# Kernel tuning notes

Hardware: AMD Instinct MI355X
Metric: run time of the kernel (lower is better)

The kernel has to match this reference:

```python
import jax, jax.numpy as jnp
import numpy as np

B, IN, H = 4096, 1024, 1024

def setup_inputs() -> dict:
    key = jax.random.key(0)
    ks = jax.random.split(key, 8)
    s = 1.0 / np.sqrt(IN + H)  # ~torch Linear init scale
    return {
        "x": jax.random.normal(ks[0], (B, IN), jnp.float32),
        "h_prev": jax.random.normal(ks[1], (B, H), jnp.float32),
        "c_prev": jax.random.normal(ks[2], (B, H), jnp.float32),
        "Wf": jax.random.normal(ks[3], (IN + H, H), jnp.float32) * s,
        "bf": jnp.zeros((H,), jnp.float32),
        "Wi": jax.random.normal(ks[4], (IN + H, H), jnp.float32) * s,
        "bi": jnp.zeros((H,), jnp.float32),
        "Wg": jax.random.normal(ks[5], (IN + H, H), jnp.float32) * s,
        "bg": jnp.zeros((H,), jnp.float32),
        "Wo": jax.random.normal(ks[6], (IN + H, H), jnp.float32) * s,
        "bo": jnp.zeros((H,), jnp.float32),
    }

def reference(x, h_prev, c_prev, Wf, bf, Wi, bi, Wg, bg, Wo, bo):
    combined = jnp.concatenate([x, h_prev], axis=1)          # [B, IN+H]
    # fuse the 4 gate projections into one GEMM: [B, IN+H] x [IN+H, 4H]
    W = jnp.concatenate([Wf, Wi, Wg, Wo], axis=1)            # [IN+H, 4H]
    b = jnp.concatenate([bf, bi, bg, bo], axis=0)            # [4H]
    gates = combined @ W + b                                  # [B, 4H]
    f_t, i_t, g_t, o_t = jnp.split(gates, 4, axis=1)
    f_t = jax.nn.sigmoid(f_t)
    i_t = jax.nn.sigmoid(i_t)
    g_t = jnp.tanh(g_t)
    o_t = jax.nn.sigmoid(o_t)
    c_next = f_t * c_prev + i_t * g_t
    h_next = o_t * jnp.tanh(c_next)
    return (h_next, c_next)
```

## Files before the change

### kernel.cpp

```cpp
#include <hip/hip_runtime.h>

#define B_DIM 4096
#define H_DIM 1024
#define K_DIM 2048

typedef unsigned short u16;
typedef unsigned int u32;
typedef __attribute__((ext_vector_type(8))) short short8;
typedef __attribute__((ext_vector_type(4))) float f32x4;

typedef const __attribute__((address_space(1))) void* gas_ptr;
typedef __attribute__((address_space(3))) void* las_ptr;

#define WT_ELEMS (4 * H_DIM * K_DIM)
#define AC_ELEMS (B_DIM * K_DIM)
#define WS_NEEDED ((size_t)(WT_ELEMS + AC_ELEMS) * 2)

__device__ __forceinline__ void gl_lds16(const u16* g, u16* l) {
    __builtin_amdgcn_global_load_lds((gas_ptr)g, (las_ptr)l, 16, 0, 0);
}
__device__ __forceinline__ float bf2f(u16 v) {
    return __builtin_bit_cast(float, (u32)((u32)v << 16));
}
__device__ __forceinline__ u16 f2bf(float f) {
    u32 u = __builtin_bit_cast(u32, f);
    return (u16)((u + 0x7fffu + ((u >> 16) & 1u)) >> 16);
}
__device__ __forceinline__ float sigm(float x) { return 1.0f / (1.0f + __expf(-x)); }
__device__ __forceinline__ float tanh_f(float x) { return 1.0f - 2.0f / (__expf(2.0f * x) + 1.0f); }

__global__ __launch_bounds__(256) void prep_a(const float* __restrict__ x, const float* __restrict__ h,
                                              u16* __restrict__ A) {
    int gid = blockIdx.x * 256 + threadIdx.x;
    int e = gid * 8;
    int m = e >> 11, c = e & 2047;
    const float* src = (c < 1024) ? (x + (size_t)m * 1024 + c) : (h + (size_t)m * 1024 + (c - 1024));
    float4 v0 = ((const float4*)src)[0], v1 = ((const float4*)src)[1];
    short8 q;
    q[0] = (short)f2bf(v0.x); q[1] = (short)f2bf(v0.y); q[2] = (short)f2bf(v0.z); q[3] = (short)f2bf(v0.w);
    q[4] = (short)f2bf(v1.x); q[5] = (short)f2bf(v1.y); q[6] = (short)f2bf(v1.z); q[7] = (short)f2bf(v1.w);
    *(short8*)(A + e) = q;
}

__global__ __launch_bounds__(256) void prep_w(const float* __restrict__ Wf, const float* __restrict__ Wi,
                                              const float* __restrict__ Wg, const float* __restrict__ Wo,
                                              u16* __restrict__ Wt) {
    __shared__ u16 tl[64][72];
    const int t = threadIdx.x;
    const int k0 = blockIdx.x * 64, n0 = blockIdx.y * 64, g = blockIdx.z;
    const float* W = (g == 0) ? Wf : (g == 1) ? Wi : (g == 2) ? Wg : Wo;
    {
        int kl = t >> 2, nc = (t & 3) * 16;
        const float4* src = (const float4*)(W + (size_t)(k0 + kl) * H_DIM + n0 + nc);
        float4 v0 = src[0], v1 = src[1], v2 = src[2], v3 = src[3];
        short8 q0, q1;
        q0[0] = (short)f2bf(v0.x); q0[1] = (short)f2bf(v0.y); q0[2] = (short)f2bf(v0.z); q0[3] = (short)f2bf(v0.w);
        q0[4] = (short)f2bf(v1.x); q0[5] = (short)f2bf(v1.y); q0[6] = (short)f2bf(v1.z); q0[7] = (short)f2bf(v1.w);
        q1[0] = (short)f2bf(v2.x); q1[1] = (short)f2bf(v2.y); q1[2] = (short)f2bf(v2.z); q1[3] = (short)f2bf(v2.w);
        q1[4] = (short)f2bf(v3.x); q1[5] = (short)f2bf(v3.y); q1[6] = (short)f2bf(v3.z); q1[7] = (short)f2bf(v3.w);
        *(short8*)&tl[kl][nc] = q0;
        *(short8*)&tl[kl][nc + 8] = q1;
    }
    __syncthreads();
    {
        int nl = t >> 2, kc = (t & 3) * 16;
        short8 r0, r1;
#pragma unroll
        for (int j = 0; j < 8; ++j) { r0[j] = (short)tl[kc + j][nl]; r1[j] = (short)tl[kc + 8 + j][nl]; }
        u16* dst = Wt + (size_t)g * (H_DIM * K_DIM) + (size_t)(n0 + nl) * K_DIM + k0 + kc;
        *(short8*)dst = r0;
        *(short8*)(dst + 8) = r1;
    }
}

__global__ __launch_bounds__(256) void lstm_gemm(
    const u16* __restrict__ A, const u16* __restrict__ Wt, const float* __restrict__ c_prev,
    const float* __restrict__ bf_, const float* __restrict__ bi_,
    const float* __restrict__ bg_, const float* __restrict__ bo_,
    float* __restrict__ out) {
    __shared__ u16 sA[256 * 64];
    __shared__ u16 sB[4 * 16 * 64];

    const int t = threadIdx.x;
    const int w = t >> 6;
    const int l = t & 63;
    const int quad = l >> 4;
    const int l15 = l & 15;
    const int m0 = blockIdx.x * 256;
    const int j0 = blockIdx.y * 16;

    f32x4 acc[4][4];
#pragma unroll
    for (int g = 0; g < 4; ++g)
#pragma unroll
        for (int mi = 0; mi < 4; ++mi)
            acc[g][mi] = (f32x4){0.f, 0.f, 0.f, 0.f};

    const int v7 = l15 & 7;

    for (int kt = 0; kt < K_DIM / 64; ++kt) {
        __syncthreads();
#pragma unroll
        for (int i = 0; i < 8; ++i) {
            int c = i * 256 + t;
            int m = c >> 3, slot = c & 7;
            int k8 = (slot ^ (m & 7)) * 8;
            gl_lds16(A + (size_t)(m0 + m) * K_DIM + kt * 64 + k8, sA + c * 8);
        }
#pragma unroll
        for (int i = 0; i < 2; ++i) {
            int c = i * 256 + t;
            int g = c >> 7, r = c & 127;
            int n = r >> 3, slot = r & 7;
            int k8 = (slot ^ (n & 7)) * 8;
            gl_lds16(Wt + (size_t)g * (H_DIM * K_DIM) + (size_t)(j0 + n) * K_DIM + kt * 64 + k8,
                     sB + c * 8);
        }
        __syncthreads();

#pragma unroll
        for (int s = 0; s < 2; ++s) {
            const int sl = ((s * 4 + quad) ^ v7) * 8;
            short8 bfr[4];
#pragma unroll
            for (int g = 0; g < 4; ++g)
                bfr[g] = *(const short8*)(sB + g * 1024 + l15 * 64 + sl);
            short8 afr[4];
#pragma unroll
            for (int mi = 0; mi < 4; ++mi)
                afr[mi] = *(const short8*)(sA + (w * 64 + mi * 16 + l15) * 64 + sl);
#pragma unroll
            for (int g = 0; g < 4; ++g)
#pragma unroll
                for (int mi = 0; mi < 4; ++mi)
                    acc[g][mi] = __builtin_amdgcn_mfma_f32_16x16x32_bf16(afr[mi], bfr[g], acc[g][mi], 0, 0, 0);
        }
    }

    const int col = j0 + l15;
    const float bF = bf_[col], bI = bi_[col], bG = bg_[col], bO = bo_[col];
#pragma unroll
    for (int mi = 0; mi < 4; ++mi) {
        const int rowbase = m0 + w * 64 + mi * 16 + quad * 4;
        float cp[4];
#pragma unroll
        for (int rr = 0; rr < 4; ++rr)
            cp[rr] = c_prev[(size_t)(rowbase + rr) * H_DIM + col];
#pragma unroll
        for (int rr = 0; rr < 4; ++rr) {
            float fv = sigm(acc[0][mi][rr] + bF);
            float iv = sigm(acc[1][mi][rr] + bI);
            float gv = tanh_f(acc[2][mi][rr] + bG);
            float ov = sigm(acc[3][mi][rr] + bO);
            float cn = fv * cp[rr] + iv * gv;
            float hn = ov * tanh_f(cn);
            size_t idx = (size_t)(rowbase + rr) * H_DIM + col;
            out[idx] = hn;
            out[(size_t)B_DIM * H_DIM + idx] = cn;
        }
    }
}

__global__ __launch_bounds__(256) void lstm_f32(
    const float* __restrict__ x, const float* __restrict__ h_prev, const float* __restrict__ c_prev,
    const float* __restrict__ Wf, const float* __restrict__ Wi, const float* __restrict__ Wg, const float* __restrict__ Wo,
    const float* __restrict__ bf_, const float* __restrict__ bi_, const float* __restrict__ bg_, const float* __restrict__ bo_,
    float* __restrict__ out) {
    __shared__ u16 smem[16384];
    u16* sA = smem;
    u16* sB = smem + 4096;

    const int t = threadIdx.x;
    const int w = t >> 6;
    const int l = t & 63;
    const int quad = l >> 4;
    const int l15 = l & 15;
    const int wr = w >> 1;
    const int wc = w & 1;
    const int m0 = blockIdx.x * 128;
    const int j0 = blockIdx.y * 32;

    const int arow = t >> 1;
    const int akh = (t & 1) * 16;
    const int r7 = t & 127;
    const int bk = r7 >> 2;
    const int bn8 = (r7 & 3) * 8;
    const int kswz = ((((bk >> 3) ^ (bn8 >> 3)) << 3) | (bk & 7));
    const float* WpA = (t < 128) ? Wf : Wi;
    const float* WpB = (t < 128) ? Wg : Wo;
    const int gA = (t >> 7);
    const int gB = 2 + (t >> 7);

    f32x4 acc[2][4][2];
#pragma unroll
    for (int gi = 0; gi < 2; ++gi)
#pragma unroll
        for (int mi = 0; mi < 4; ++mi)
#pragma unroll
            for (int ni = 0; ni < 2; ++ni)
                acc[gi][mi][ni] = (f32x4){0.f, 0.f, 0.f, 0.f};

    for (int kt = 0; kt < K_DIM / 32; ++kt) {
        const float* srcA = (kt < 32) ? x : h_prev;
        const int koff = (kt & 31) * 32;
        __syncthreads();

        const float4* ap = (const float4*)(srcA + (size_t)(m0 + arow) * H_DIM + koff + akh);
        float4 a0 = ap[0], a1 = ap[1], a2 = ap[2], a3 = ap[3];
        short8 p0, p1;
        p0[0] = (short)f2bf(a0.x); p0[1] = (short)f2bf(a0.y); p0[2] = (short)f2bf(a0.z); p0[3] = (short)f2bf(a0.w);
        p0[4] = (short)f2bf(a1.x); p0[5] = (short)f2bf(a1.y); p0[6] = (short)f2bf(a1.z); p0[7] = (short)f2bf(a1.w);
        p1[0] = (short)f2bf(a2.x); p1[1] = (short)f2bf(a2.y); p1[2] = (short)f2bf(a2.z); p1[3] = (short)f2bf(a2.w);
        p1[4] = (short)f2bf(a3.x); p1[5] = (short)f2bf(a3.y); p1[6] = (short)f2bf(a3.z); p1[7] = (short)f2bf(a3.w);
        *(short8*)(sA + arow * 32 + akh) = p0;
        *(short8*)(sA + arow * 32 + akh + 8) = p1;

        const float* gpA = WpA + (size_t)(kt * 32 + bk) * H_DIM + j0 + bn8;
        const float* gpB = WpB + (size_t)(kt * 32 + bk) * H_DIM + j0 + bn8;
        float4 c0 = *(const float4*)gpA, c1 = *(const float4*)(gpA + 4);
        float4 d0 = *(const float4*)gpB, d1 = *(const float4*)(gpB + 4);
        sB[gA * 1024 + (bn8 + 0) * 32 + kswz] = f2bf(c0.x);
        sB[gA * 1024 + (bn8 + 1) * 32 + kswz] = f2bf(c0.y);
        sB[gA * 1024 + (bn8 + 2) * 32 + kswz] = f2bf(c0.z);
        sB[gA * 1024 + (bn8 + 3) * 32 + kswz] = f2bf(c0.w);
        sB[gA * 1024 + (bn8 + 4) * 32 + kswz] = f2bf(c1.x);
        sB[gA * 1024 + (bn8 + 5) * 32 + kswz] = f2bf(c1.y);
        sB[gA * 1024 + (bn8 + 6) * 32 + kswz] = f2bf(c1.z);
        sB[gA * 1024 + (bn8 + 7) * 32 + kswz] = f2bf(c1.w);
        sB[gB * 1024 + (bn8 + 0) * 32 + kswz] = f2bf(d0.x);
        sB[gB * 1024 + (bn8 + 1) * 32 + kswz] = f2bf(d0.y);
        sB[gB * 1024 + (bn8 + 2) * 32 + kswz] = f2bf(d0.z);
        sB[gB * 1024 + (bn8 + 3) * 32 + kswz] = f2bf(d0.w);
        sB[gB * 1024 + (bn8 + 4) * 32 + kswz] = f2bf(d1.x);
        sB[gB * 1024 + (bn8 + 5) * 32 + kswz] = f2bf(d1.y);
        sB[gB * 1024 + (bn8 + 6) * 32 + kswz] = f2bf(d1.z);
        sB[gB * 1024 + (bn8 + 7) * 32 + kswz] = f2bf(d1.w);
        __syncthreads();

        short8 bfr[2][2];
#pragma unroll
        for (int gi = 0; gi < 2; ++gi) {
            int g = wc * 2 + gi;
#pragma unroll
            for (int ni = 0; ni < 2; ++ni) {
                int n = ni * 16 + l15;
                bfr[gi][ni] = *(const short8*)(sB + g * 1024 + n * 32 + ((quad ^ (n >> 3)) * 8));
            }
        }
#pragma unroll
        for (int mi = 0; mi < 4; ++mi) {
            int m = wr * 64 + mi * 16 + l15;
            short8 afr = *(const short8*)(sA + m * 32 + quad * 8);
#pragma unroll
            for (int gi = 0; gi < 2; ++gi)
#pragma unroll
                for (int ni = 0; ni < 2; ++ni)
                    acc[gi][mi][ni] =
                        __builtin_amdgcn_mfma_f32_16x16x32_bf16(afr, bfr[gi][ni], acc[gi][mi][ni], 0, 0, 0);
        }
    }

    __syncthreads();
#pragma unroll
    for (int gi = 0; gi < 2; ++gi) {
        int g = wc * 2 + gi;
        const float* bp = (g == 0) ? bf_ : (g == 1) ? bi_ : (g == 2) ? bg_ : bo_;
#pragma unroll
        for (int ni = 0; ni < 2; ++ni) {
            int col = ni * 16 + l15;
            float bias = bp[j0 + col];
#pragma unroll
            for (int mi = 0; mi < 4; ++mi)
#pragma unroll
                for (int rr = 0; rr < 4; ++rr) {
                    int row = wr * 64 + mi * 16 + quad * 4 + rr;
                    float v = acc[gi][mi][ni][rr] + bias;
                    v = (g == 2) ? tanh_f(v) : sigm(v);
                    smem[g * 4096 + row * 32 + col] = f2bf(v);
                }
        }
    }
    __syncthreads();

    const int col = t & 31;
    const int rb = t >> 5;
#pragma unroll
    for (int p = 0; p < 16; ++p) {
        int row = p * 8 + rb;
        float fv = bf2f(smem[0 * 4096 + row * 32 + col]);
        float iv = bf2f(smem[1 * 4096 + row * 32 + col]);
        float gv = bf2f(smem[2 * 4096 + row * 32 + col]);
        float ov = bf2f(smem[3 * 4096 + row * 32 + col]);
        size_t oidx = (size_t)(m0 + row) * H_DIM + j0 + col;
        float cp = c_prev[oidx];
        float cn = fv * cp + iv * gv;
        float hn = ov * tanh_f(cn);
        out[oidx] = hn;
        out[(size_t)B_DIM * H_DIM + oidx] = cn;
    }
}

extern "C" void kernel_launch(void* const* d_in, const int* in_sizes, int n_in,
                              void* d_out, int out_size, void* d_ws, size_t ws_size,
                              hipStream_t stream) {
    const float* x   = (const float*)d_in[0];
    const float* hp  = (const float*)d_in[1];
    const float* cp  = (const float*)d_in[2];
    const float* Wf  = (const float*)d_in[3];
    const float* bf_ = (const float*)d_in[4];
    const float* Wi  = (const float*)d_in[5];
    const float* bi_ = (const float*)d_in[6];
    const float* Wg  = (const float*)d_in[7];
    const float* bg_ = (const float*)d_in[8];
    const float* Wo  = (const float*)d_in[9];
    const float* bo_ = (const float*)d_in[10];

    if (ws_size >= WS_NEEDED) {
        u16* Wt = (u16*)d_ws;
        u16* Ac = (u16*)d_ws + WT_ELEMS;
        prep_a<<<dim3(AC_ELEMS / 8 / 256), dim3(256), 0, stream>>>(x, hp, Ac);
        prep_w<<<dim3(K_DIM / 64, H_DIM / 64, 4), dim3(256), 0, stream>>>(Wf, Wi, Wg, Wo, Wt);
        lstm_gemm<<<dim3(B_DIM / 256, H_DIM / 16), dim3(256), 0, stream>>>(
            Ac, Wt, cp, bf_, bi_, bg_, bo_, (float*)d_out);
    } else {
        lstm_f32<<<dim3(B_DIM / 128, H_DIM / 32), dim3(256), 0, stream>>>(
            x, hp, cp, Wf, Wi, Wg, Wo, bf_, bi_, bg_, bo_, (float*)d_out);
    }
}
```

Baseline: 224.4 us.

## Reshape GEMM tile to 128x32 with 2x2 wave grid and merge prep kernels

The LSTM GEMM block tile changes from 256 rows x 16 columns per gate to 128 rows x 32 columns per gate, with the four waves arranged 2x2. This balances A and B reuse and lowers global/LDS traffic per output. Per-thread load pointers are precomputed and incremented each k-step, removing index arithmetic from the loop. The two conversion kernels for activations and weights are merged into one launch, cutting launch overhead and tail gaps.

```diff
diff --git a/kernel.cpp b/kernel.cpp
--- a/kernel.cpp
+++ b/kernel.cpp
@@ -29,47 +29,47 @@
 __device__ __forceinline__ float sigm(float x) { return 1.0f / (1.0f + __expf(-x)); }
 __device__ __forceinline__ float tanh_f(float x) { return 1.0f - 2.0f / (__expf(2.0f * x) + 1.0f); }
 
-__global__ __launch_bounds__(256) void prep_a(const float* __restrict__ x, const float* __restrict__ h,
-                                              u16* __restrict__ A) {
-    int gid = blockIdx.x * 256 + threadIdx.x;
-    int e = gid * 8;
-    int m = e >> 11, c = e & 2047;
-    const float* src = (c < 1024) ? (x + (size_t)m * 1024 + c) : (h + (size_t)m * 1024 + (c - 1024));
-    float4 v0 = ((const float4*)src)[0], v1 = ((const float4*)src)[1];
-    short8 q;
-    q[0] = (short)f2bf(v0.x); q[1] = (short)f2bf(v0.y); q[2] = (short)f2bf(v0.z); q[3] = (short)f2bf(v0.w);
-    q[4] = (short)f2bf(v1.x); q[5] = (short)f2bf(v1.y); q[6] = (short)f2bf(v1.z); q[7] = (short)f2bf(v1.w);
-    *(short8*)(A + e) = q;
-}
-
-__global__ __launch_bounds__(256) void prep_w(const float* __restrict__ Wf, const float* __restrict__ Wi,
-                                              const float* __restrict__ Wg, const float* __restrict__ Wo,
-                                              u16* __restrict__ Wt) {
+__global__ __launch_bounds__(256) void prep_all(const float* __restrict__ x, const float* __restrict__ h,
+                                                const float* __restrict__ Wf, const float* __restrict__ Wi,
+                                                const float* __restrict__ Wg, const float* __restrict__ Wo,
+                                                u16* __restrict__ A, u16* __restrict__ Wt) {
     __shared__ u16 tl[64][72];
     const int t = threadIdx.x;
-    const int k0 = blockIdx.x * 64, n0 = blockIdx.y * 64, g = blockIdx.z;
-    const float* W = (g == 0) ? Wf : (g == 1) ? Wi : (g == 2) ? Wg : Wo;
-    {
-        int kl = t >> 2, nc = (t & 3) * 16;
-        const float4* src = (const float4*)(W + (size_t)(k0 + kl) * H_DIM + n0 + nc);
-        float4 v0 = src[0], v1 = src[1], v2 = src[2], v3 = src[3];
-        short8 q0, q1;
-        q0[0] = (short)f2bf(v0.x); q0[1] = (short)f2bf(v0.y); q0[2] = (short)f2bf(v0.z); q0[3] = (short)f2bf(v0.w);
-        q0[4] = (short)f2bf(v1.x); q0[5] = (short)f2bf(v1.y); q0[6] = (short)f2bf(v1.z); q0[7] = (short)f2bf(v1.w);
-        q1[0] = (short)f2bf(v2.x); q1[1] = (short)f2bf(v2.y); q1[2] = (short)f2bf(v2.z); q1[3] = (short)f2bf(v2.w);
-        q1[4] = (short)f2bf(v3.x); q1[5] = (short)f2bf(v3.y); q1[6] = (short)f2bf(v3.z); q1[7] = (short)f2bf(v3.w);
-        *(short8*)&tl[kl][nc] = q0;
-        *(short8*)&tl[kl][nc + 8] = q1;
-    }
-    __syncthreads();
-    {
-        int nl = t >> 2, kc = (t & 3) * 16;
-        short8 r0, r1;
-#pragma unroll
-        for (int j = 0; j < 8; ++j) { r0[j] = (short)tl[kc + j][nl]; r1[j] = (short)tl[kc + 8 + j][nl]; }
-        u16* dst = Wt + (size_t)g * (H_DIM * K_DIM) + (size_t)(n0 + nl) * K_DIM + k0 + kc;
-        *(short8*)dst = r0;
-        *(short8*)(dst + 8) = r1;
+    if (blockIdx.x < 4096) {
+        int e = (blockIdx.x * 256 + t) * 8;
+        int m = e >> 11, c = e & 2047;
+        const float* src = (c < 1024) ? (x + (size_t)m * 1024 + c) : (h + (size_t)m * 1024 + (c - 1024));
+        float4 v0 = ((const float4*)src)[0], v1 = ((const float4*)src)[1];
+        short8 q;
+        q[0] = (short)f2bf(v0.x); q[1] = (short)f2bf(v0.y); q[2] = (short)f2bf(v0.z); q[3] = (short)f2bf(v0.w);
+        q[4] = (short)f2bf(v1.x); q[5] = (short)f2bf(v1.y); q[6] = (short)f2bf(v1.z); q[7] = (short)f2bf(v1.w);
+        *(short8*)(A + e) = q;
+    } else {
+        int bid = blockIdx.x - 4096;
+        const int k0 = (bid & 31) * 64, n0 = ((bid >> 5) & 15) * 64, g = bid >> 9;
+        const float* W = (g == 0) ? Wf : (g == 1) ? Wi : (g == 2) ? Wg : Wo;
+        {
+            int kl = t >> 2, nc = (t & 3) * 16;
+            const float4* src = (const float4*)(W + (size_t)(k0 + kl) * H_DIM + n0 + nc);
+            float4 v0 = src[0], v1 = src[1], v2 = src[2], v3 = src[3];
+            short8 q0, q1;
+            q0[0] = (short)f2bf(v0.x); q0[1] = (short)f2bf(v0.y); q0[2] = (short)f2bf(v0.z); q0[3] = (short)f2bf(v0.w);
+            q0[4] = (short)f2bf(v1.x); q0[5] = (short)f2bf(v1.y); q0[6] = (short)f2bf(v1.z); q0[7] = (short)f2bf(v1.w);
+            q1[0] = (short)f2bf(v2.x); q1[1] = (short)f2bf(v2.y); q1[2] = (short)f2bf(v2.z); q1[3] = (short)f2bf(v2.w);
+            q1[4] = (short)f2bf(v3.x); q1[5] = (short)f2bf(v3.y); q1[6] = (short)f2bf(v3.z); q1[7] = (short)f2bf(v3.w);
+            *(short8*)&tl[kl][nc] = q0;
+            *(short8*)&tl[kl][nc + 8] = q1;
+        }
+        __syncthreads();
+        {
+            int nl = t >> 2, kc = (t & 3) * 16;
+            short8 r0, r1;
+#pragma unroll
+            for (int j = 0; j < 8; ++j) { r0[j] = (short)tl[kc + j][nl]; r1[j] = (short)tl[kc + 8 + j][nl]; }
+            u16* dst = Wt + (size_t)g * (H_DIM * K_DIM) + (size_t)(n0 + nl) * K_DIM + k0 + kc;
+            *(short8*)dst = r0;
+            *(short8*)(dst + 8) = r1;
+        }
     }
 }
 
@@ -78,16 +78,18 @@
     const float* __restrict__ bf_, const float* __restrict__ bi_,
     const float* __restrict__ bg_, const float* __restrict__ bo_,
     float* __restrict__ out) {
-    __shared__ u16 sA[256 * 64];
-    __shared__ u16 sB[4 * 16 * 64];
+    __shared__ u16 sA[128 * 64];
+    __shared__ u16 sB[4 * 32 * 64];
 
     const int t = threadIdx.x;
     const int w = t >> 6;
     const int l = t & 63;
     const int quad = l >> 4;
     const int l15 = l & 15;
-    const int m0 = blockIdx.x * 256;
-    const int j0 = blockIdx.y * 16;
+    const int wr = w >> 1;
+    const int wc = w & 1;
+    const int m0 = blockIdx.x * 128;
+    const int j0 = blockIdx.y * 32;
 
     f32x4 acc[4][4];
 #pragma unroll
@@ -96,25 +98,34 @@
         for (int mi = 0; mi < 4; ++mi)
             acc[g][mi] = (f32x4){0.f, 0.f, 0.f, 0.f};
 
+    const u16* pA[4];
+    const u16* pB[4];
+#pragma unroll
+    for (int i = 0; i < 4; ++i) {
+        int c = i * 256 + t;
+        int m = c >> 3, slot = c & 7;
+        pA[i] = A + (size_t)(m0 + m) * K_DIM + (slot ^ (m & 7)) * 8;
+    }
+#pragma unroll
+    for (int i = 0; i < 4; ++i) {
+        int c = i * 256 + t;
+        int g = c >> 8, r = c & 255;
+        int n = r >> 3, slot = r & 7;
+        pB[i] = Wt + (size_t)g * (H_DIM * K_DIM) + (size_t)(j0 + n) * K_DIM + (slot ^ (n & 7)) * 8;
+    }
     const int v7 = l15 & 7;
 
     for (int kt = 0; kt < K_DIM / 64; ++kt) {
         __syncthreads();
 #pragma unroll
-        for (int i = 0; i < 8; ++i) {
-            int c = i * 256 + t;
-            int m = c >> 3, slot = c & 7;
-            int k8 = (slot ^ (m & 7)) * 8;
-            gl_lds16(A + (size_t)(m0 + m) * K_DIM + kt * 64 + k8, sA + c * 8);
-        }
-#pragma unroll
-        for (int i = 0; i < 2; ++i) {
-            int c = i * 256 + t;
-            int g = c >> 7, r = c & 127;
-            int n = r >> 3, slot = r & 7;
-            int k8 = (slot ^ (n & 7)) * 8;
-            gl_lds16(Wt + (size_t)g * (H_DIM * K_DIM) + (size_t)(j0 + n) * K_DIM + kt * 64 + k8,
-                     sB + c * 8);
+        for (int i = 0; i < 4; ++i) {
+            gl_lds16(pA[i], sA + (i * 256 + t) * 8);
+            pA[i] += 64;
+        }
+#pragma unroll
+        for (int i = 0; i < 4; ++i) {
+            gl_lds16(pB[i], sB + (i * 256 + t) * 8);
+            pB[i] += 64;
         }
         __syncthreads();
 
@@ -124,11 +135,11 @@
             short8 bfr[4];
 #pragma unroll
             for (int g = 0; g < 4; ++g)
-                bfr[g] = *(const short8*)(sB + g * 1024 + l15 * 64 + sl);
+                bfr[g] = *(const short8*)(sB + g * 2048 + (wc * 16 + l15) * 64 + sl);
             short8 afr[4];
 #pragma unroll
             for (int mi = 0; mi < 4; ++mi)
-                afr[mi] = *(const short8*)(sA + (w * 64 + mi * 16 + l15) * 64 + sl);
+                afr[mi] = *(const short8*)(sA + (wr * 64 + mi * 16 + l15) * 64 + sl);
 #pragma unroll
             for (int g = 0; g < 4; ++g)
 #pragma unroll
@@ -137,11 +148,11 @@
         }
     }
 
-    const int col = j0 + l15;
+    const int col = j0 + wc * 16 + l15;
     const float bF = bf_[col], bI = bi_[col], bG = bg_[col], bO = bo_[col];
 #pragma unroll
     for (int mi = 0; mi < 4; ++mi) {
-        const int rowbase = m0 + w * 64 + mi * 16 + quad * 4;
+        const int rowbase = m0 + wr * 64 + mi * 16 + quad * 4;
         float cp[4];
 #pragma unroll
         for (int rr = 0; rr < 4; ++rr)
@@ -318,9 +329,8 @@
     if (ws_size >= WS_NEEDED) {
         u16* Wt = (u16*)d_ws;
         u16* Ac = (u16*)d_ws + WT_ELEMS;
-        prep_a<<<dim3(AC_ELEMS / 8 / 256), dim3(256), 0, stream>>>(x, hp, Ac);
-        prep_w<<<dim3(K_DIM / 64, H_DIM / 64, 4), dim3(256), 0, stream>>>(Wf, Wi, Wg, Wo, Wt);
-        lstm_gemm<<<dim3(B_DIM / 256, H_DIM / 16), dim3(256), 0, stream>>>(
+        prep_all<<<dim3(4096 + 2048), dim3(256), 0, stream>>>(x, hp, Wf, Wi, Wg, Wo, Ac, Wt);
+        lstm_gemm<<<dim3(B_DIM / 128, H_DIM / 32), dim3(256), 0, stream>>>(
             Ac, Wt, cp, bf_, bi_, bg_, bo_, (float*)d_out);
     } else {
         lstm_f32<<<dim3(B_DIM / 128, H_DIM / 32), dim3(256), 0, stream>>>(
```

New measurement: 211.9 us. -5.6%, faster.
